# Optimization experiments

Hardware: AMD Instinct MI355X
Metric: run time of the kernel (lower is better)

## Reference

```python
import jax, jax.numpy as jnp
import numpy as np

B, T, D, U = 64, 512, 1024, 1024


def hard_sigmoid(x):
    # keras hard_sigmoid: clip(0.2*x + 0.5, 0, 1)
    return jnp.clip(0.2 * x + 0.5, 0.0, 1.0)


def setup_inputs() -> dict:
    key = jax.random.key(0)
    ks = jax.random.split(key, 6)
    x = jax.random.normal(ks[0], (B, T, D), jnp.float32)
    # glorot-ish scaled params
    kernel = jax.random.normal(ks[1], (D, 4 * U), jnp.float32) * (1.0 / np.sqrt(D).astype(np.float32))
    recurrent_kernel = jax.random.normal(ks[2], (U, 4 * U), jnp.float32) * (1.0 / np.sqrt(U).astype(np.float32))
    peephole_kernel = jax.random.normal(ks[3], (U, 3 * U), jnp.float32) * (1.0 / np.sqrt(U).astype(np.float32))
    projection_kernel = jax.random.normal(ks[4], (U, U), jnp.float32) * (1.0 / np.sqrt(U).astype(np.float32))
    # unit_forget_bias: [zeros(U), ones(U), zeros(2U)] for (i, f, c, o)
    bias = jnp.concatenate([jnp.zeros((U,), jnp.float32), jnp.ones((U,), jnp.float32), jnp.zeros((2 * U,), jnp.float32)])
    h0 = jnp.zeros((B, U), jnp.float32)
    c0 = jnp.zeros((B, U), jnp.float32)
    return {"x": x, "h0": h0, "c0": c0, "kernel": kernel, "recurrent_kernel": recurrent_kernel,
            "peephole_kernel": peephole_kernel, "projection_kernel": projection_kernel, "bias": bias}


def reference(x, h0, c0, kernel, recurrent_kernel, peephole_kernel, projection_kernel, bias):
    U_ = h0.shape[-1]
    Pi = peephole_kernel[:, :U_]
    Pf = peephole_kernel[:, U_:2 * U_]
    Po = peephole_kernel[:, 2 * U_:3 * U_]

    def step(carry, x_t):
        h, c = carry
        # fused gate pre-activations: [B, 4U]
        z = x_t @ kernel + h @ recurrent_kernel + bias
        zi, zf, zc, zo = jnp.split(z, 4, axis=-1)
        i = hard_sigmoid(zi + c @ Pi)            # input gate w/ peephole on c_{t-1}
        f = hard_sigmoid(zf + c @ Pf)            # forget gate w/ peephole on c_{t-1}
        c_new = f * c + i * jnp.tanh(zc)
        o = hard_sigmoid(zo + c_new @ Po)        # output gate w/ peephole on c_t
        # residual LSTM: project tanh(c_t), add residual input, gate by o
        h_new = o * (jnp.tanh(c_new) @ projection_kernel + x_t)
        return (h_new, c_new), h_new

    xs = jnp.swapaxes(x, 0, 1)  # [T, B, D]
    (_, _), hs = jax.lax.scan(step, (h0, c0), xs)
    return jnp.swapaxes(hs, 0, 1)  # [B, T, U]
```

## Files before the change

### kernel.cpp

```cpp
#include <hip/hip_runtime.h>
#include <cstdint>
#include <cstddef>

#define NB 64
#define NT 512
#define ND 1024
#define NU 1024

typedef short s16x8 __attribute__((ext_vector_type(8)));
typedef float f32x4 __attribute__((ext_vector_type(4)));
typedef unsigned int u32x2 __attribute__((ext_vector_type(2)));
typedef unsigned int u32x4 __attribute__((ext_vector_type(4)));
typedef unsigned short u16;

__device__ __forceinline__ u16 f2bf(float f) {
  unsigned int u = __float_as_uint(f);
  u += 0x7fffu + ((u >> 16) & 1u);
  return (u16)(u >> 16);
}
__device__ __forceinline__ float bf2f(u16 s) {
  return __uint_as_float(((unsigned int)s) << 16);
}
__device__ __forceinline__ float hsig(float x) {
  return fminf(fmaxf(0.2f * x + 0.5f, 0.0f), 1.0f);
}
__device__ __forceinline__ float ftanh(float x) {
  float e = __expf(2.0f * x);
  return 1.0f - 2.0f / (e + 1.0f);
}
__device__ __forceinline__ f32x4 mfma16(s16x8 a, s16x8 b, f32x4 c) {
  return __builtin_amdgcn_mfma_f32_16x16x32_bf16(a, b, c, 0, 0, 0);
}

__device__ __forceinline__ void atomic_swap_u32(unsigned int* p, unsigned int v) {
  asm volatile("global_atomic_swap %0, %1, off" :: "v"(p), "v"(v) : "memory");
}
__device__ __forceinline__ void atomic_swap_u64(unsigned int* p, u32x2 v) {
  asm volatile("global_atomic_swap_x2 %0, %1, off" :: "v"(p), "v"(v) : "memory");
}

template <int STAGED>
__device__ __forceinline__ void ldx4(s16x8& d, const u16* a) {
  if constexpr (STAGED)
    asm volatile("global_load_dwordx4 %0, %1, off" : "=v"(d) : "v"(a));
  else
    asm volatile("global_load_dwordx4 %0, %1, off sc0 sc1" : "=v"(d) : "v"(a));
}

#define WAIT_VM0() do { \
    asm volatile("s_waitcnt vmcnt(0)" ::: "memory"); \
    __builtin_amdgcn_sched_barrier(0); \
  } while (0)

__global__ __launch_bounds__(256) void wt_cvt(const float* __restrict__ W,
                                              u16* __restrict__ Wt) {
  __shared__ u16 T[64][65];
  const int tid = threadIdx.x;
  const int k0 = (blockIdx.x & 15) * 64;
  const int n0 = (blockIdx.x >> 4) * 64;
  const int r = tid >> 2, c4 = (tid & 3) * 16;
  {
    const float* src = W + (size_t)(k0 + r) * 4096 + n0 + c4;
#pragma unroll
    for (int j = 0; j < 4; ++j) {
      float4 v = ((const float4*)src)[j];
      T[r][c4 + j * 4 + 0] = f2bf(v.x); T[r][c4 + j * 4 + 1] = f2bf(v.y);
      T[r][c4 + j * 4 + 2] = f2bf(v.z); T[r][c4 + j * 4 + 3] = f2bf(v.w);
    }
  }
  __syncthreads();
  {
    u16 tmp[16];
#pragma unroll
    for (int i = 0; i < 16; ++i) tmp[i] = T[c4 + i][r];
    u16* dst = Wt + (size_t)(n0 + r) * 1024 + k0 + c4;
    *(s16x8*)dst = *(s16x8*)tmp;
    *(s16x8*)(dst + 8) = *(s16x8*)(tmp + 8);
  }
}

template <int WT>
__global__ __launch_bounds__(256) void xw_gemm(const float* __restrict__ X,
                                               const float* __restrict__ W,
                                               const u16* __restrict__ Wt,
                                               u16* __restrict__ XW) {
  __shared__ u16 Al[128][72];
  __shared__ u16 Bl[128][72];
  const int tid = threadIdx.x;
  const int lane = tid & 63;
  const int wv = tid >> 6;
  const int m0 = (blockIdx.x >> 5) * 128;
  const int n0 = (blockIdx.x & 31) * 128;
  f32x4 acc[4][4];
#pragma unroll
  for (int i = 0; i < 4; ++i)
#pragma unroll
    for (int j = 0; j < 4; ++j) acc[i][j] = (f32x4){0.f, 0.f, 0.f, 0.f};

  for (int kt = 0; kt < 1024; kt += 64) {
    {
      const int r = tid >> 1, hh = (tid & 1) * 32;
      const float* src = X + (size_t)(m0 + r) * 1024 + kt + hh;
      u16* dst = &Al[r][hh];
      if constexpr (WT) {
#pragma unroll
        for (int j = 0; j < 4; ++j) {
          float4 v0 = ((const float4*)src)[2 * j];
          float4 v1 = ((const float4*)src)[2 * j + 1];
          u32x4 q;
          q[0] = ((unsigned)f2bf(v0.y) << 16) | f2bf(v0.x);
          q[1] = ((unsigned)f2bf(v0.w) << 16) | f2bf(v0.z);
          q[2] = ((unsigned)f2bf(v1.y) << 16) | f2bf(v1.x);
          q[3] = ((unsigned)f2bf(v1.w) << 16) | f2bf(v1.z);
          *(u32x4*)(dst + j * 8) = q;
        }
      } else {
#pragma unroll
        for (int j = 0; j < 8; ++j) {
          float4 v = ((const float4*)src)[j];
          dst[j * 4 + 0] = f2bf(v.x); dst[j * 4 + 1] = f2bf(v.y);
          dst[j * 4 + 2] = f2bf(v.z); dst[j * 4 + 3] = f2bf(v.w);
        }
      }
    }
    if constexpr (WT) {
      const int n = tid >> 1, kh = (tid & 1) * 32;
      const u16* src = Wt + (size_t)(n0 + n) * 1024 + kt + kh;
      u16* dst = &Bl[n][kh];
#pragma unroll
      for (int j = 0; j < 4; ++j)
        *(s16x8*)(dst + j * 8) = *(const s16x8*)(src + j * 8);
    } else {
      const int kr = tid >> 2, q = (tid & 3) * 32;
      const float* src = W + (size_t)(kt + kr) * 4096 + n0 + q;
#pragma unroll
      for (int j = 0; j < 8; ++j) {
        float4 v = ((const float4*)src)[j];
        const int n = q + j * 4;
        Bl[n + 0][kr] = f2bf(v.x); Bl[n + 1][kr] = f2bf(v.y);
        Bl[n + 2][kr] = f2bf(v.z); Bl[n + 3][kr] = f2bf(v.w);
      }
    }
    __syncthreads();
    const int wm = (wv >> 1) * 64, wn = (wv & 1) * 64;
    const int row = lane & 15, kq = (lane >> 4) * 8;
#pragma unroll
    for (int ks = 0; ks < 2; ++ks) {
      s16x8 af[4], bq[4];
#pragma unroll
      for (int i = 0; i < 4; ++i) af[i] = *(const s16x8*)&Al[wm + i * 16 + row][ks * 32 + kq];
#pragma unroll
      for (int j = 0; j < 4; ++j) bq[j] = *(const s16x8*)&Bl[wn + j * 16 + row][ks * 32 + kq];
#pragma unroll
      for (int i = 0; i < 4; ++i)
#pragma unroll
        for (int j = 0; j < 4; ++j) acc[i][j] = mfma16(af[i], bq[j], acc[i][j]);
    }
    __syncthreads();
  }
  const int wm = (wv >> 1) * 64, wn = (wv & 1) * 64;
  const int col16 = lane & 15, rq = (lane >> 4) * 4;
#pragma unroll
  for (int i = 0; i < 4; ++i)
#pragma unroll
    for (int j = 0; j < 4; ++j)
#pragma unroll
      for (int q = 0; q < 4; ++q) {
        const int m = m0 + wm + i * 16 + rq + q;
        const int n = n0 + wn + j * 16 + col16;
        const int t = m & 511, b = m >> 9;
        const int g = n >> 10, uu = n & 1023;
        const int ugrp = uu >> 3, ul2 = uu & 7;
        XW[(((size_t)ugrp * 512 + t) * 64 + b) * 32 + ul2 * 4 + g] = f2bf(acc[i][j][q]);
      }
}

__global__ void init_comm(const float* __restrict__ h0, const float* __restrict__ c0,
                          u16* hini, u16* cini) {
  const int i = blockIdx.x * 256 + threadIdx.x;
  hini[i] = f2bf(h0[i]);
  cini[i] = f2bf(c0[i]);
}

__device__ __forceinline__ void gbar(unsigned int* flags, int bid, int tid, unsigned int ep) {
  __syncthreads();
  if (tid == 0) atomic_swap_u32(flags + bid * 16, ep);
  unsigned int* f = flags + ((((tid & 127) << 1) | (bid & 1)) * 16);
  for (;;) {
    unsigned int v;
    asm volatile("global_load_dword %0, %1, off sc0 sc1\n\ts_waitcnt vmcnt(0)"
                 : "=v"(v) : "v"(f) : "memory");
    if (v >= ep) break;
    __builtin_amdgcn_s_sleep(1);
  }
  __syncthreads();
}

#define WLDS_B   (64 * 1032 * 2)
#define ZOFF     WLDS_B
#define POFF     (ZOFF + 32 * 34 * 4)
#define OOFF     (POFF + 32 * 17 * 4)
#define SMEM_B   (OOFF + 32 * 17 * 4)
#define STEP_E   65536

template <int STAGED>
__global__ __launch_bounds__(256, 1) void lstm_loop(
    const float* __restrict__ rec, const float* __restrict__ peep,
    const float* __restrict__ projw, const float* __restrict__ bias,
    const float* __restrict__ x, const u16* __restrict__ xw,
    float* __restrict__ out,
    u16* hini, u16* cini, u16* thsg,
    u16* hst, u16* cst, u16* thst,
    unsigned int* flags, const float* __restrict__ c0) {
  extern __shared__ char smem[];
  u16 (*wlds)[1032] = (u16(*)[1032])smem;
  float (*zlds)[34] = (float(*)[34])(smem + ZOFF);
  float (*plds)[17] = (float(*)[17])(smem + POFF);
  float (*olds)[17] = (float(*)[17])(smem + OOFF);

  const int tid = threadIdx.x;
  const int lane = tid & 63;
  const int wv = tid >> 6;
  const int bid = blockIdx.x;
  const int ugrp = bid >> 1;
  const int row0 = (bid & 1) * 32;
  const int u0 = ugrp * 8;

  for (int g = 0; g < 8; ++g) {
    const int c = g * 8 + (tid & 3) * 2;
    const float* sp; int stride, scol;
    if (c < 32)      { sp = rec;   stride = 4096; scol = (c >> 3) * 1024 + u0 + (c & 7); }
    else if (c < 48) { sp = peep;  stride = 3072; scol = ((c - 32) >> 3) * 1024 + u0 + (c & 7); }
    else if (c < 56) { sp = peep;  stride = 3072; scol = 2048 + u0 + (c & 7); }
    else             { sp = projw; stride = 1024; scol = u0 + (c - 56); }
#pragma unroll 4
    for (int p = 0; p < 16; ++p) {
      const int k = p * 64 + (tid >> 2);
      float2 v = *(const float2*)(sp + (size_t)k * stride + scol);
      wlds[c][k] = f2bf(v.x);
      wlds[c + 1][k] = f2bf(v.y);
    }
  }

  const int r = tid >> 3;
  const int ul = tid & 7;
  const int brow = row0 + r;
  const int u = u0 + ul;
  const float b_i = bias[u], b_f = bias[1024 + u], b_c = bias[2048 + u], b_o = bias[3072 + u];
  float cstv = c0[brow * 1024 + u];

  const int fcol = lane & 15;
  const int kofs = (lane >> 4) * 8;

  s16x8 av[32];
  u32x2 xwp;
  float xp;

  {
    const u16* xr0 = xw + (((size_t)ugrp * 512 + 0) * 64 + brow) * 32 + ul * 4;
    asm volatile("global_load_dwordx2 %0, %1, off" : "=v"(xwp) : "v"(xr0));
    const float* xs0 = x + (size_t)brow * (512 * 1024) + u;
    asm volatile("global_load_dword %0, %1, off" : "=v"(xp) : "v"(xs0));
  }
  if (wv < 2) {
    const u16* ap = cini + (size_t)(row0 + wv * 16 + fcol) * 1024 + kofs;
#pragma unroll
    for (int kt = 0; kt < 32; ++kt)
      asm volatile("global_load_dwordx4 %0, %1, off sc0 sc1"
                   : "=v"(av[kt]) : "v"(ap + kt * 32));
  }
  WAIT_VM0();
  __syncthreads();

  for (int t = 0; t < NT; ++t) {
    float zo_reg, xres, hv;
    const size_t xo = (size_t)brow * (512 * 1024) + (size_t)t * 1024 + u;

    const u16* hsrc; u16* cpub; u16* thpub; const u16* csrc; const u16* thsrc; u16* hpub;
    if constexpr (STAGED) {
      hsrc  = t ? (hst + (size_t)(t - 1) * STEP_E) : hini;
      hpub  = hst + (size_t)t * STEP_E;
      cpub  = cst + (size_t)t * STEP_E;   csrc  = cpub;
      thpub = thst + (size_t)t * STEP_E;  thsrc = thpub;
    } else {
      hsrc = hini; hpub = hini; cpub = cini; csrc = cini; thpub = thsg; thsrc = thsg;
    }

    if (wv >= 2) {
      const int rt = wv - 2;
      const u16* ap = hsrc + (size_t)(row0 + rt * 16 + fcol) * 1024 + kofs;
#pragma unroll
      for (int kt = 0; kt < 32; ++kt) ldx4<STAGED>(av[kt], ap + kt * 32);
      WAIT_VM0();
      f32x4 accA = {0.f, 0.f, 0.f, 0.f}, accB = {0.f, 0.f, 0.f, 0.f};
      const u16* bp0 = &wlds[fcol][kofs];
      const u16* bp1 = &wlds[16 + fcol][kofs];
#pragma unroll
      for (int kt = 0; kt < 32; ++kt) {
        accA = mfma16(av[kt], *(const s16x8*)(bp0 + kt * 32), accA);
        accB = mfma16(av[kt], *(const s16x8*)(bp1 + kt * 32), accB);
      }
      const int srow = rt * 16 + (lane >> 4) * 4;
#pragma unroll
      for (int q = 0; q < 4; ++q) {
        zlds[srow + q][fcol] = accA[q];
        zlds[srow + q][16 + fcol] = accB[q];
      }
    } else {
      f32x4 accP = {0.f, 0.f, 0.f, 0.f};
      const u16* bp = &wlds[32 + fcol][kofs];
#pragma unroll
      for (int kt = 0; kt < 32; ++kt)
        accP = mfma16(av[kt], *(const s16x8*)(bp + kt * 32), accP);
      const int srow = wv * 16 + (lane >> 4) * 4;
#pragma unroll
      for (int q = 0; q < 4; ++q) plds[srow + q][fcol] = accP[q];
    }
    __syncthreads();
    {
      const float xw_i = bf2f((u16)(xwp[0] & 0xffffu));
      const float xw_f = bf2f((u16)(xwp[0] >> 16));
      const float xw_c = bf2f((u16)(xwp[1] & 0xffffu));
      const float xw_o = bf2f((u16)(xwp[1] >> 16));
      xres = xp;
      const float zi = zlds[r][ul]      + xw_i + b_i + plds[r][ul];
      const float zf = zlds[r][8 + ul]  + xw_f + b_f + plds[r][8 + ul];
      const float zc = zlds[r][16 + ul] + xw_c + b_c;
      zo_reg         = zlds[r][24 + ul] + xw_o + b_o;
      const float ig = hsig(zi), fg = hsig(zf);
      cstv = fg * cstv + ig * ftanh(zc);
      const float th = ftanh(cstv);
      const unsigned int cb = f2bf(cstv), tb = f2bf(th);
      const unsigned int cp = ((unsigned)__shfl_xor((int)cb, 1) << 16) | cb;
      const unsigned int tp = ((unsigned)__shfl_xor((int)tb, 1) << 16) | tb;
      const unsigned int cp2 = (unsigned)__shfl_xor((int)cp, 2);
      const unsigned int tp2 = (unsigned)__shfl_xor((int)tp, 2);
      if ((ul & 3) == 0) {
        u32x2 cq; cq[0] = cp; cq[1] = cp2;
        u32x2 tq; tq[0] = tp; tq[1] = tp2;
        atomic_swap_u64((unsigned int*)(cpub + brow * 1024 + u), cq);
        atomic_swap_u64((unsigned int*)(thpub + brow * 1024 + u), tq);
      }
    }
    WAIT_VM0();
    gbar(flags, bid, tid, 2 * t + 1);

    {
      const int prt = wv & 1;
      const u16* ap = ((wv < 2) ? csrc : thsrc)
                      + (size_t)(row0 + prt * 16 + fcol) * 1024 + kofs;
#pragma unroll
      for (int kt = 0; kt < 32; ++kt) ldx4<STAGED>(av[kt], ap + kt * 32);
      {
        const int tn = (t + 1 < NT) ? (t + 1) : t;
        const u16* xrn = xw + (((size_t)ugrp * 512 + tn) * 64 + brow) * 32 + ul * 4;
        asm volatile("global_load_dwordx2 %0, %1, off" : "=v"(xwp) : "v"(xrn));
        const float* xsn = x + (size_t)brow * (512 * 1024) + (size_t)tn * 1024 + u;
        asm volatile("global_load_dword %0, %1, off" : "=v"(xp) : "v"(xsn));
      }
      asm volatile("s_waitcnt vmcnt(2)" ::: "memory");
      __builtin_amdgcn_sched_barrier(0);
      f32x4 acc = {0.f, 0.f, 0.f, 0.f};
      const u16* bp = &wlds[48 + fcol][kofs];
#pragma unroll
      for (int kt = 0; kt < 32; ++kt)
        acc = mfma16(av[kt], *(const s16x8*)(bp + kt * 32), acc);
      const int srow = prt * 16 + (lane >> 4) * 4;
      if (wv < 2) {
        if (fcol < 8) {
#pragma unroll
          for (int q = 0; q < 4; ++q) olds[srow + q][fcol] = acc[q];
        }
      } else {
        if (fcol >= 8) {
#pragma unroll
          for (int q = 0; q < 4; ++q) olds[srow + q][fcol] = acc[q];
        }
      }
    }
    __syncthreads();
    {
      const float og = hsig(zo_reg + olds[r][ul]);
      const float pv = olds[r][8 + ul] + xres;
      hv = og * pv;
      const unsigned int hb = f2bf(hv);
      const unsigned int hp = ((unsigned)__shfl_xor((int)hb, 1) << 16) | hb;
      const unsigned int hp2 = (unsigned)__shfl_xor((int)hp, 2);
      if ((ul & 3) == 0) {
        u32x2 hq; hq[0] = hp; hq[1] = hp2;
        atomic_swap_u64((unsigned int*)(hpub + brow * 1024 + u), hq);
      }
    }
    WAIT_VM0();
    gbar(flags, bid, tid, 2 * t + 2);
    asm volatile("global_store_dword %0, %1, off" :: "v"(out + xo), "v"(hv) : "memory");
  }
}

extern "C" void kernel_launch(void* const* d_in, const int* in_sizes, int n_in,
                              void* d_out, int out_size, void* d_ws, size_t ws_size,
                              hipStream_t stream) {
  const float* x    = (const float*)d_in[0];
  const float* h0   = (const float*)d_in[1];
  const float* c0   = (const float*)d_in[2];
  const float* W    = (const float*)d_in[3];
  const float* R    = (const float*)d_in[4];
  const float* P    = (const float*)d_in[5];
  const float* PRJ  = (const float*)d_in[6];
  const float* bias = (const float*)d_in[7];
  float* out = (float*)d_out;
  char* ws = (char*)d_ws;

  const size_t XW_BYTES = (size_t)32768 * 4096 * 2;
  size_t off = XW_BYTES;
  u16* xw   = (u16*)ws;
  u16* hini = (u16*)(ws + off); off += 131072;
  u16* cini = (u16*)(ws + off); off += 131072;
  u16* thsg = (u16*)(ws + off); off += 131072;
  unsigned int* flags = (unsigned int*)(ws + off); off += 16384;
  const size_t base_need = off;
  u16* hst = (u16*)(ws + off); off += (size_t)NT * 131072;
  u16* cst = (u16*)(ws + off); off += (size_t)NT * 131072;
  u16* thst = (u16*)(ws + off); off += (size_t)NT * 131072;
  const size_t staged_need = off;
  u16* Wt = (u16*)(ws + off); off += (size_t)4096 * 1024 * 2;
  const size_t wt_need = off;
  if (ws_size < base_need) return;
  const int staged = (ws_size >= staged_need) ? 1 : 0;
  const int wt = (ws_size >= wt_need) ? 1 : 0;

  (void)hipFuncSetAttribute(reinterpret_cast<const void*>(&lstm_loop<1>),
                            hipFuncAttributeMaxDynamicSharedMemorySize, 160 * 1024);
  (void)hipFuncSetAttribute(reinterpret_cast<const void*>(&lstm_loop<0>),
                            hipFuncAttributeMaxDynamicSharedMemorySize, 160 * 1024);

  hipMemsetAsync(flags, 0, 16384, stream);
  hipLaunchKernelGGL(init_comm, dim3(256), dim3(256), 0, stream, h0, c0, hini, cini);
  if (wt) {
    hipLaunchKernelGGL(wt_cvt, dim3(1024), dim3(256), 0, stream, W, Wt);
    hipLaunchKernelGGL((xw_gemm<1>), dim3(8192), dim3(256), 0, stream, x, W, Wt, xw);
  } else {
    hipLaunchKernelGGL((xw_gemm<0>), dim3(8192), dim3(256), 0, stream, x, W, Wt, xw);
  }

  void* args[15];
  args[0] = (void*)&R;     args[1] = (void*)&P;     args[2] = (void*)&PRJ;
  args[3] = (void*)&bias;  args[4] = (void*)&x;     args[5] = (void*)&xw;
  args[6] = (void*)&out;   args[7] = (void*)&hini;  args[8] = (void*)&cini;
  args[9] = (void*)&thsg;  args[10] = (void*)&hst;  args[11] = (void*)&cst;
  args[12] = (void*)&thst; args[13] = (void*)&flags; args[14] = (void*)&c0;

  const void* fn = staged ? (const void*)&lstm_loop<1> : (const void*)&lstm_loop<0>;
  hipError_t e = hipLaunchCooperativeKernel(fn, dim3(256), dim3(256),
                                            args, (unsigned int)SMEM_B, stream);
  if (e != hipSuccess) {
    if (staged)
      hipLaunchKernelGGL((lstm_loop<1>), dim3(256), dim3(256), SMEM_B, stream,
                         R, P, PRJ, bias, x, xw, out, hini, cini, thsg,
                         hst, cst, thst, flags, c0);
    else
      hipLaunchKernelGGL((lstm_loop<0>), dim3(256), dim3(256), SMEM_B, stream,
                         R, P, PRJ, bias, x, xw, out, hini, cini, thsg,
                         hst, cst, thst, flags, c0);
  }
}
```

Before: 7.035 ms.

## Split grid barrier into arrive/poll so peephole waves skip the h-barrier wait

The second grid barrier of each step is split into an arrive and a deferred poll. Only the waves that consume h (the recurrent GEMM waves) now wait for the step-end barrier, while the peephole waves start immediately on data they already hold. The next-step xw/x prefetch and the output store move to after the h publish, the second-half pollers are staggered with a sleep, and the LDS scratch stride is widened. The goal is to shorten the critical path of each recurrent step, at the cost of relying on subtle memory ordering via partial vmcnt waits.

New measurement: 6.958 ms. Within noise of the previous version (-1.1%).

```diff
diff --git a/kernel.cpp b/kernel.cpp
--- a/kernel.cpp
+++ b/kernel.cpp
@@ -49,6 +49,10 @@
 
 #define WAIT_VM0() do { \
     asm volatile("s_waitcnt vmcnt(0)" ::: "memory"); \
+    __builtin_amdgcn_sched_barrier(0); \
+  } while (0)
+#define WAIT_VM(N) do { \
+    asm volatile("s_waitcnt vmcnt(" #N ")" ::: "memory"); \
     __builtin_amdgcn_sched_barrier(0); \
   } while (0)
 
@@ -182,10 +186,15 @@
   cini[i] = f2bf(c0[i]);
 }
 
-__device__ __forceinline__ void gbar(unsigned int* flags, int bid, int tid, unsigned int ep) {
+__device__ __forceinline__ void gbar_arrive(unsigned int* flags, int bid, int tid,
+                                            unsigned int ep) {
   __syncthreads();
   if (tid == 0) atomic_swap_u32(flags + bid * 16, ep);
+}
+__device__ __forceinline__ void gbar_poll(unsigned int* flags, int bid, int tid,
+                                          unsigned int ep, int stagger) {
   unsigned int* f = flags + ((((tid & 127) << 1) | (bid & 1)) * 16);
+  if (stagger && (tid & 128)) __builtin_amdgcn_s_sleep(7);
   for (;;) {
     unsigned int v;
     asm volatile("global_load_dword %0, %1, off sc0 sc1\n\ts_waitcnt vmcnt(0)"
@@ -193,14 +202,14 @@
     if (v >= ep) break;
     __builtin_amdgcn_s_sleep(1);
   }
-  __syncthreads();
 }
 
 #define WLDS_B   (64 * 1032 * 2)
+#define SCR_S    44
 #define ZOFF     WLDS_B
-#define POFF     (ZOFF + 32 * 34 * 4)
-#define OOFF     (POFF + 32 * 17 * 4)
-#define SMEM_B   (OOFF + 32 * 17 * 4)
+#define POFF     (ZOFF + 32 * SCR_S * 4)
+#define OOFF     (POFF + 32 * SCR_S * 4)
+#define SMEM_B   (OOFF + 32 * SCR_S * 4)
 #define STEP_E   65536
 
 template <int STAGED>
@@ -214,9 +223,9 @@
     unsigned int* flags, const float* __restrict__ c0) {
   extern __shared__ char smem[];
   u16 (*wlds)[1032] = (u16(*)[1032])smem;
-  float (*zlds)[34] = (float(*)[34])(smem + ZOFF);
-  float (*plds)[17] = (float(*)[17])(smem + POFF);
-  float (*olds)[17] = (float(*)[17])(smem + OOFF);
+  float (*zlds)[SCR_S] = (float(*)[SCR_S])(smem + ZOFF);
+  float (*plds)[SCR_S] = (float(*)[SCR_S])(smem + POFF);
+  float (*olds)[SCR_S] = (float(*)[SCR_S])(smem + OOFF);
 
   const int tid = threadIdx.x;
   const int lane = tid & 63;
@@ -287,6 +296,7 @@
     }
 
     if (wv >= 2) {
+      gbar_poll(flags, bid, tid, 2 * (unsigned)t, 0);
       const int rt = wv - 2;
       const u16* ap = hsrc + (size_t)(row0 + rt * 16 + fcol) * 1024 + kofs;
 #pragma unroll
@@ -315,6 +325,7 @@
       const int srow = wv * 16 + (lane >> 4) * 4;
 #pragma unroll
       for (int q = 0; q < 4; ++q) plds[srow + q][fcol] = accP[q];
+      WAIT_VM(1);
     }
     __syncthreads();
     {
@@ -343,7 +354,9 @@
       }
     }
     WAIT_VM0();
-    gbar(flags, bid, tid, 2 * t + 1);
+    gbar_arrive(flags, bid, tid, 2 * t + 1);
+    gbar_poll(flags, bid, tid, 2 * t + 1, 1);
+    __syncthreads();
 
     {
       const int prt = wv & 1;
@@ -351,15 +364,7 @@
                       + (size_t)(row0 + prt * 16 + fcol) * 1024 + kofs;
 #pragma unroll
       for (int kt = 0; kt < 32; ++kt) ldx4<STAGED>(av[kt], ap + kt * 32);
-      {
-        const int tn = (t + 1 < NT) ? (t + 1) : t;
-        const u16* xrn = xw + (((size_t)ugrp * 512 + tn) * 64 + brow) * 32 + ul * 4;
-        asm volatile("global_load_dwordx2 %0, %1, off" : "=v"(xwp) : "v"(xrn));
-        const float* xsn = x + (size_t)brow * (512 * 1024) + (size_t)tn * 1024 + u;
-        asm volatile("global_load_dword %0, %1, off" : "=v"(xp) : "v"(xsn));
-      }
-      asm volatile("s_waitcnt vmcnt(2)" ::: "memory");
-      __builtin_amdgcn_sched_barrier(0);
+      WAIT_VM0();
       f32x4 acc = {0.f, 0.f, 0.f, 0.f};
       const u16* bp = &wlds[48 + fcol][kofs];
 #pragma unroll
@@ -390,10 +395,15 @@
         u32x2 hq; hq[0] = hp; hq[1] = hp2;
         atomic_swap_u64((unsigned int*)(hpub + brow * 1024 + u), hq);
       }
-    }
-    WAIT_VM0();
-    gbar(flags, bid, tid, 2 * t + 2);
-    asm volatile("global_store_dword %0, %1, off" :: "v"(out + xo), "v"(hv) : "memory");
+      const int tn = (t + 1 < NT) ? (t + 1) : t;
+      const u16* xrn = xw + (((size_t)ugrp * 512 + tn) * 64 + brow) * 32 + ul * 4;
+      asm volatile("global_load_dwordx2 %0, %1, off" : "=v"(xwp) : "v"(xrn));
+      const float* xsn = x + (size_t)brow * (512 * 1024) + (size_t)tn * 1024 + u;
+      asm volatile("global_load_dword %0, %1, off" : "=v"(xp) : "v"(xsn));
+      asm volatile("global_store_dword %0, %1, off" :: "v"(out + xo), "v"(hv) : "memory");
+      WAIT_VM(3);
+    }
+    gbar_arrive(flags, bid, tid, 2 * t + 2);
   }
 }
 
```
